# Optimization experiments

Measured on AMD Instinct MI355X. Metric: run time of the kernel, lower is better.

The kernel has to match this reference:

```python
import jax, jax.numpy as jnp
import numpy as np
from math import factorial, sqrt, pi

LMAX, NSH = 2, 9
F = 64
N_RBF = 20
N_INTER = 2
N_ATOMS = 1000
N_PAIRS = 10000
CUTOFF = 5.0

# ---------- Clebsch-Gordan coefficients for real spherical harmonics ----------

def _cg_complex(l1, m1, l2, m2, l3, m3):
    # <l1 m1 l2 m2 | l3 m3> via Racah formula
    if m3 != m1 + m2 or not (abs(l1 - l2) <= l3 <= l1 + l2):
        return 0.0
    f = factorial
    pre = sqrt((2 * l3 + 1) * f(l3 + l1 - l2) * f(l3 - l1 + l2) * f(l1 + l2 - l3) / f(l1 + l2 + l3 + 1))
    pre *= sqrt(f(l3 + m3) * f(l3 - m3) * f(l1 - m1) * f(l1 + m1) * f(l2 - m2) * f(l2 + m2))
    s = 0.0
    for k in range(l1 + l2 - l3 + 1):
        d = [k, l1 + l2 - l3 - k, l1 - m1 - k, l2 + m2 - k, l3 - l2 + m1 + k, l3 - l1 - m2 + k]
        if min(d) < 0:
            continue
        s += (-1) ** k / np.prod([float(f(t)) for t in d])
    return pre * s

def _sh_indices(lmax):
    l = np.concatenate([np.full(2 * ll + 1, ll) for ll in range(lmax + 1)])
    m = np.concatenate([np.arange(-ll, ll + 1) for ll in range(lmax + 1)])
    return l, m

def _real_cg(lmax):
    lidx, midx = _sh_indices(lmax)
    n = (lmax + 1) ** 2
    cgc = np.zeros((n, n, n))
    for a in range(n):
        for b in range(n):
            for c in range(n):
                cgc[a, b, c] = _cg_complex(lidx[a], midx[a], lidx[b], midx[b], lidx[c], midx[c])
    # complex -> real spherical harmonic change of basis (per degree l)
    U = np.zeros((n, n), dtype=np.complex128)
    for ll in range(lmax + 1):
        base = ll * ll + ll
        U[base, base] = 1.0
        for m in range(1, ll + 1):
            U[base + m, base - m] = 1 / sqrt(2)
            U[base + m, base + m] = (-1) ** m / sqrt(2)
            U[base - m, base - m] = 1j / sqrt(2)
            U[base - m, base + m] = -1j * (-1) ** m / sqrt(2)
    cgr = np.einsum('ijk,ai,bj,ck->abc', cgc.astype(np.complex128), U, U, U.conj())
    parity = (-1.0) ** lidx
    mask = (parity[:, None, None] * parity[None, :, None]) == parity[None, None, :]
    cgr = np.real(cgr) * mask
    cgr = np.transpose(cgr, (2, 0, 1))  # [s_out, s_in(x), s_filter(Y)]
    s1, s2, s3 = np.nonzero(np.abs(cgr) > 1e-9)
    return s1, s2, s3, cgr[s1, s2, s3].astype(np.float32), lidx

_S1, _S2, _S3, _CGV, _LIDX = _real_cg(LMAX)
IDX1 = jnp.asarray(_S1)            # output sh channel per CG path
IDX2 = jnp.asarray(_S2)            # input-feature sh channel per CG path
IDX3 = jnp.asarray(_S3)            # Ylm sh channel per CG path
CGVAL = jnp.asarray(_CGV)          # CG value per path
WIDX = jnp.asarray(_LIDX[_S3])     # radial-filter degree per CG path
LIDX = jnp.asarray(_LIDX)          # degree of each of the 9 sh channels

# ---------- real spherical harmonics (lmax=2, orthonormal, m=-l..l order) ----------

def _rsh(u):
    x, y, z = u[:, 0], u[:, 1], u[:, 2]
    c1 = sqrt(3.0 / (4.0 * pi))
    c2 = 0.5 * sqrt(15.0 / pi)
    return jnp.stack([
        jnp.full_like(x, 0.5 / sqrt(pi)),
        c1 * y, c1 * z, c1 * x,
        c2 * x * y,
        c2 * y * z,
        0.25 * sqrt(5.0 / pi) * (3.0 * z * z - 1.0),
        c2 * x * z,
        0.25 * sqrt(15.0 / pi) * (x * x - y * y),
    ], axis=1)


def setup_inputs() -> dict:
    key = jax.random.key(0)
    ks = jax.random.split(key, 10)
    atomic_numbers = jax.random.randint(ks[0], (N_ATOMS,), 0, 100)
    r_ij = 1.5 * jax.random.normal(ks[1], (N_PAIRS, 3), dtype=jnp.float32)
    idx_i = jnp.sort(jax.random.randint(ks[2], (N_PAIRS,), 0, N_ATOMS))
    idx_j = jax.random.randint(ks[3], (N_PAIRS,), 0, N_ATOMS)
    emb = jax.random.normal(ks[4], (100, F), dtype=jnp.float32)
    def s(k, sh, fan):
        return jax.random.normal(k, sh, dtype=jnp.float32) / float(np.sqrt(fan))
    Wf = s(ks[5], (N_INTER, N_RBF, (LMAX + 1) * F), N_RBF)
    bf = jnp.zeros((N_INTER, (LMAX + 1) * F), jnp.float32)
    W1 = s(ks[6], (N_INTER, F, F), F)
    W2 = s(ks[7], (N_INTER, F, F), F)
    W3 = s(ks[8], (N_INTER, F, F), F)
    Wg = s(ks[9], (N_INTER, F, (LMAX + 1) * F), F)
    bg = jnp.zeros((N_INTER, (LMAX + 1) * F), jnp.float32)
    return dict(atomic_numbers=atomic_numbers, r_ij=r_ij, idx_i=idx_i, idx_j=idx_j,
                emb=emb, Wf=Wf, bf=bf, W1=W1, W2=W2, W3=W3, Wg=Wg, bg=bg)


def reference(atomic_numbers, r_ij, idx_i, idx_j, emb, Wf, bf, W1, W2, W3, Wg, bg):
    n_atoms = atomic_numbers.shape[0]
    d = jnp.linalg.norm(r_ij, axis=1, keepdims=True)          # [P,1]
    Yij = _rsh(r_ij / d)                                       # [P,9]
    offsets = jnp.linspace(0.0, CUTOFF, N_RBF)                 # GaussianRBF
    width = CUTOFF / (N_RBF - 1)
    radial = jnp.exp((-0.5 / (width * width)) * (d - offsets) ** 2)   # [P,n_rbf]
    cut = 0.5 * (jnp.cos(d * (pi / CUTOFF)) + 1.0) * (d < CUTOFF)     # [P,1]
    # nuclear embedding + scalar2rsh (zero-pad l>0 channels)
    x = jnp.zeros((n_atoms, NSH, F), emb.dtype).at[:, 0, :].set(emb[atomic_numbers])
    for t in range(N_INTER):
        # SO3Convolution
        Wij = (radial @ Wf[t] + bf[t]).reshape(-1, LMAX + 1, F) * cut[:, :, None]  # [P,lmax+1,F]
        xj = x[idx_j]                                                              # [P,9,F]
        v = xj[:, IDX2] * Yij[:, IDX3, None] * Wij[:, WIDX] * CGVAL[None, :, None]  # [P,nnz,F]
        yij = jnp.zeros_like(xj).at[:, IDX1].add(v)                                 # CG scatter
        dx = jax.ops.segment_sum(yij, idx_i, num_segments=n_atoms)                  # edge->node scatter
        # mixing1 + SO3TensorProduct
        ddx = dx @ W1[t]
        tp = jnp.zeros_like(dx).at[:, IDX1].add(dx[:, IDX2] * ddx[:, IDX3] * CGVAL[None, :, None])
        dx = (dx + tp) @ W2[t]
        # SO3ParametricGatedNonlinearity (gate from l=0 channel)
        gate = (dx[:, 0] @ Wg[t] + bg[t]).reshape(-1, LMAX + 1, F)
        dx = dx * jax.nn.sigmoid(gate[:, LIDX])
        dx = dx @ W3[t]
        x = x + dx
    return x  # multipole_representation [n_atoms, 9, F]; x[:,0] is scalar_representation
```

## Files before the change

### kernel.cpp

```cpp
#include <hip/hip_runtime.h>
#include <cmath>

constexpr int kNsh    = 9;
constexpr int kF      = 64;
constexpr int kNrbf   = 20;
constexpr int kNAtoms = 1000;
constexpr int kNPairs = 10000;
constexpr float kCutoffF = 5.0f;
constexpr int kMaxNZ  = 200;
constexpr int kCp     = 12;
constexpr int kXs     = kF * kCp;

struct CGSparse {
  int n;
  int c[kMaxNZ];
  int a[kMaxNZ];
  int b[kMaxNZ];
  float v[kMaxNZ];
};

constexpr double cfact(int n) {
  double r = 1.0;
  for (int i = 2; i <= n; i++) r *= (double)i;
  return r;
}
constexpr double cabs_(double x) { return x < 0 ? -x : x; }
constexpr double csqrt_(double x) {
  if (x <= 0.0) return 0.0;
  double g = x < 1.0 ? 1.0 : x;
  for (int i = 0; i < 60; i++) g = 0.5 * (g + x / g);
  return g;
}

constexpr double cg_cplx(int l1, int m1, int l2, int m2, int l3, int m3) {
  if (m3 != m1 + m2) return 0.0;
  int lo = l1 > l2 ? l1 - l2 : l2 - l1;
  if (l3 < lo || l3 > l1 + l2) return 0.0;
  double pre = csqrt_((2 * l3 + 1) * cfact(l3 + l1 - l2) * cfact(l3 - l1 + l2) *
                      cfact(l1 + l2 - l3) / cfact(l1 + l2 + l3 + 1));
  pre *= csqrt_(cfact(l3 + m3) * cfact(l3 - m3) * cfact(l1 - m1) *
                cfact(l1 + m1) * cfact(l2 - m2) * cfact(l2 + m2));
  double s = 0.0;
  for (int k = 0; k <= l1 + l2 - l3; k++) {
    int d0 = k, d1 = l1 + l2 - l3 - k, d2 = l1 - m1 - k;
    int d3 = l2 + m2 - k, d4 = l3 - l2 + m1 + k, d5 = l3 - l1 - m2 + k;
    if (d0 < 0 || d1 < 0 || d2 < 0 || d3 < 0 || d4 < 0 || d5 < 0) continue;
    double den = cfact(d0) * cfact(d1) * cfact(d2) * cfact(d3) * cfact(d4) * cfact(d5);
    s += ((k % 2) ? -1.0 : 1.0) / den;
  }
  return pre * s;
}

constexpr CGSparse build_cg() {
  CGSparse out{};
  int lidx[9] = {0, 1, 1, 1, 2, 2, 2, 2, 2};
  int midx[9] = {0, -1, 0, 1, -2, -1, 0, 1, 2};
  double Ur[9][9] = {};
  double Ui[9][9] = {};
  for (int l = 0; l <= 2; l++) {
    int base = l * l + l;
    Ur[base][base] = 1.0;
    for (int m = 1; m <= l; m++) {
      double s2 = 1.0 / csqrt_(2.0);
      double sgn = (m % 2) ? -1.0 : 1.0;
      Ur[base + m][base - m] = s2;
      Ur[base + m][base + m] = sgn * s2;
      Ui[base - m][base - m] = s2;
      Ui[base - m][base + m] = -sgn * s2;
    }
  }
  double cgr[9][9][9] = {};
  for (int i = 0; i < 9; i++)
    for (int j = 0; j < 9; j++)
      for (int k = 0; k < 9; k++) {
        double cv = cg_cplx(lidx[i], midx[i], lidx[j], midx[j], lidx[k], midx[k]);
        if (cv == 0.0) continue;
        for (int a2 = 0; a2 < 9; a2++) {
          if (Ur[a2][i] == 0.0 && Ui[a2][i] == 0.0) continue;
          for (int b2 = 0; b2 < 9; b2++) {
            if (Ur[b2][j] == 0.0 && Ui[b2][j] == 0.0) continue;
            for (int c2 = 0; c2 < 9; c2++) {
              if (Ur[c2][k] == 0.0 && Ui[c2][k] == 0.0) continue;
              double ar = Ur[a2][i], ai = Ui[a2][i];
              double br = Ur[b2][j], bi = Ui[b2][j];
              double cr = Ur[c2][k], ci = -Ui[c2][k];
              double pr = ar * br - ai * bi;
              double pi = ar * bi + ai * br;
              double rr = pr * cr - pi * ci;
              cgr[c2][a2][b2] += rr * cv;
            }
          }
        }
      }
  int n = 0;
  for (int c2 = 0; c2 < 9; c2++)
    for (int a2 = 0; a2 < 9; a2++)
      for (int b2 = 0; b2 < 9; b2++) {
        bool mask = ((lidx[a2] + lidx[b2]) % 2) == (lidx[c2] % 2);
        double v = mask ? cgr[c2][a2][b2] : 0.0;
        if (cabs_(v) > 1e-9) {
          out.c[n] = c2;
          out.a[n] = a2;
          out.b[n] = b2;
          out.v[n] = (float)v;
          n++;
        }
      }
  out.n = n;
  return out;
}

constexpr CGSparse CG = build_cg();
static_assert(CG.n > 0 && CG.n <= kMaxNZ, "CG table size out of range");

constexpr int kPreBlkPairs = kNPairs / 4;
constexpr int kPreBlkSeg   = (kNAtoms + 1 + 255) / 256;
constexpr int kPreBlkTotal = kPreBlkPairs + kPreBlkSeg;

__global__ __launch_bounds__(256) void k_pre(
    const float* __restrict__ rij, const int* __restrict__ idx_i,
    float* __restrict__ pd_all, int* __restrict__ seg) {
  const int blk = blockIdx.x;
  if (blk < kPreBlkPairs) {
    int wv = threadIdx.x >> 6;
    int f = threadIdx.x & 63;
    int p = blk * 4 + wv;
    float rx = rij[3 * p + 0], ry = rij[3 * p + 1], rz = rij[3 * p + 2];
    float d = sqrtf(rx * rx + ry * ry + rz * rz);
    float inv = 1.0f / d;
    float x = rx * inv, y = ry * inv, z = rz * inv;
    const float c0 = 0.28209479177387814f;
    const float c1 = 0.4886025119029199f;
    const float c2 = 1.0925484305920792f;
    const float c3 = 0.31539156525252005f;
    const float c4 = 0.5462742152960396f;
    float cut = (d < kCutoffF) ? 0.5f * (cosf(d * (float)(M_PI / 5.0)) + 1.0f) : 0.0f;
    float val = 0.f;
    if (f < 9) {
      val =
          (f == 0) ? c0 :
          (f == 1) ? c1 * y :
          (f == 2) ? c1 * z :
          (f == 3) ? c1 * x :
          (f == 4) ? c2 * x * y :
          (f == 5) ? c2 * y * z :
          (f == 6) ? c3 * (3.0f * z * z - 1.0f) :
          (f == 7) ? c2 * x * z :
                     c4 * (x * x - y * y);
    } else if (f == 9) {
      val = cut;
    } else if (f < 30) {
      const float width = kCutoffF / (kNrbf - 1);
      const float coef = -0.5f / (width * width);
      float off = (kCutoffF * (f - 10)) / (kNrbf - 1);
      float tt = d - off;
      val = expf(coef * tt * tt) * cut;
    }
    if (f < 30) pd_all[p * 32 + f] = val;
  } else {
    int a = (blk - kPreBlkPairs) * 256 + threadIdx.x;
    if (a <= kNAtoms) {
      int lo = 0, hi = kNPairs;
      while (lo < hi) {
        int mid = (lo + hi) >> 1;
        if (idx_i[mid] < a) lo = mid + 1; else hi = mid;
      }
      seg[a] = lo;
    }
  }
}

__device__ __forceinline__ void mm_phase(const float* __restrict__ sIn,
                                         const float* __restrict__ W,
                                         float* __restrict__ sRw,
                                         int k0, int cgi, int fb) {
  if (cgi >= 3) return;
  const int c0 = cgi * 4;
  float acc[4][4];
  #pragma unroll
  for (int i = 0; i < 4; i++)
    #pragma unroll
    for (int j = 0; j < 4; j++) acc[i][j] = 0.f;
  #pragma unroll
  for (int half = 0; half < 2; half++) {
    float4 wr[8];
    #pragma unroll
    for (int kk = 0; kk < 8; kk++) {
      wr[kk] = *(const float4*)(W + (k0 + half * 8 + kk) * kF + fb);
    }
    #pragma unroll
    for (int kk = 0; kk < 8; kk++) {
      int k = k0 + half * 8 + kk;
      float4 av = *(const float4*)(sIn + k * kCp + c0);
      float4 wv = wr[kk];
      float a[4] = {av.x, av.y, av.z, av.w};
      float w[4] = {wv.x, wv.y, wv.z, wv.w};
      #pragma unroll
      for (int i = 0; i < 4; i++)
        #pragma unroll
        for (int j = 0; j < 4; j++) acc[i][j] += a[i] * w[j];
    }
  }
  #pragma unroll
  for (int j = 0; j < 4; j++) {
    float4 v = {acc[0][j], acc[1][j], acc[2][j], acc[3][j]};
    *(float4*)(sRw + (fb + j) * kCp + c0) = v;
  }
}

template <int T>
__global__ __launch_bounds__(256) void k_inter(
    const float* __restrict__ pd_all, const float* __restrict__ Wft,
    const float* __restrict__ bft, const int* __restrict__ seg,
    const int* __restrict__ idx_j, const int* __restrict__ Z,
    const float* __restrict__ emb, const float* __restrict__ x_in,
    const float* __restrict__ W1, const float* __restrict__ W2,
    const float* __restrict__ W3, const float* __restrict__ Wg,
    const float* __restrict__ bg, float* __restrict__ x_out) {
  const int atom = blockIdx.x;
  const int tid = threadIdx.x;
  const int wv = tid >> 6;
  const int lane = tid & 63;
  const int cgi = lane >> 4;
  const int fb = (lane & 15) * 4;
  const int k0 = wv * 16;

  __shared__ __align__(16) float sWf[kNrbf * 192];
  __shared__ __align__(16) float sA[kF * kCp];
  __shared__ __align__(16) float sR[4][kF * kCp];
  __shared__ __align__(16) float sGp[4][192];

  {
    const float4* g4 = (const float4*)Wft;
    float4* s4 = (float4*)sWf;
    #pragma unroll
    for (int r = 0; r < 4; r++) {
      int i = r * 256 + tid;
      if (i < kNrbf * 192 / 4) s4[i] = g4[i];
    }
  }
  const float bf0 = bft[lane], bf1 = bft[64 + lane], bf2 = bft[128 + lane];
  __syncthreads();

  {
    float y[12];
    #pragma unroll
    for (int c = 0; c < 12; c++) y[c] = 0.f;
    const int s0 = seg[atom], s1 = seg[atom + 1];
    for (int p0 = s0 + wv; p0 < s1; p0 += 4) {
      const int p = __builtin_amdgcn_readfirstlane(p0);
      const int j = __builtin_amdgcn_readfirstlane(idx_j[p]);
      const float* pd = pd_all + p * 32;
      const float cut = pd[9];
      float Wl0 = bf0 * cut, Wl1 = bf1 * cut, Wl2 = bf2 * cut;
      #pragma unroll
      for (int k = 0; k < kNrbf; k++) {
        float r = pd[10 + k];
        Wl0 += r * sWf[k * 192 + lane];
        Wl1 += r * sWf[k * 192 + 64 + lane];
        Wl2 += r * sWf[k * 192 + 128 + lane];
      }
      float YW[9];
      YW[0] = pd[0] * Wl0;
      YW[1] = pd[1] * Wl1;
      YW[2] = pd[2] * Wl1;
      YW[3] = pd[3] * Wl1;
      #pragma unroll
      for (int b = 4; b < 9; b++) YW[b] = pd[b] * Wl2;
      if (T == 0) {
        float e = emb[Z[j] * kF + lane];
        #pragma unroll
        for (int q = 0; q < CG.n; q++) {
          if (CG.a[q] == 0) y[CG.c[q]] += CG.v[q] * YW[CG.b[q]] * e;
        }
      } else {
        const float* xj = x_in + j * kXs + lane * kCp;
        float xv[12];
        *(float4*)&xv[0] = *(const float4*)(xj + 0);
        *(float4*)&xv[4] = *(const float4*)(xj + 4);
        *(float4*)&xv[8] = *(const float4*)(xj + 8);
        #pragma unroll
        for (int q = 0; q < CG.n; q++) {
          y[CG.c[q]] += CG.v[q] * YW[CG.b[q]] * xv[CG.a[q]];
        }
      }
    }
    float4* r4 = (float4*)(sR[wv] + lane * kCp);
    r4[0] = *(float4*)&y[0];
    r4[1] = *(float4*)&y[4];
    r4[2] = *(float4*)&y[8];
  }
  __syncthreads();
  if (tid < 192) {
    const float4* r0 = (const float4*)sR[0];
    const float4* r1 = (const float4*)sR[1];
    const float4* r2 = (const float4*)sR[2];
    const float4* r3 = (const float4*)sR[3];
    float4 a = r0[tid], b = r1[tid], c = r2[tid], d = r3[tid];
    float4 s = {a.x + b.x + c.x + d.x, a.y + b.y + c.y + d.y,
                a.z + b.z + c.z + d.z, a.w + b.w + c.w + d.w};
    ((float4*)sA)[tid] = s;
  }
  __syncthreads();

  mm_phase(sA, W1, sR[wv], k0, cgi, fb);
  __syncthreads();

  if (wv == 0) {
    float dxv[12], ddx[12];
    {
      const float4* sa = (const float4*)(sA + lane * kCp);
      *(float4*)&dxv[0] = sa[0];
      *(float4*)&dxv[4] = sa[1];
      *(float4*)&dxv[8] = sa[2];
    }
    #pragma unroll
    for (int c = 0; c < 12; c++) {
      ddx[c] = sR[0][lane * kCp + c] + sR[1][lane * kCp + c] +
               sR[2][lane * kCp + c] + sR[3][lane * kCp + c];
    }
    float t2[12];
    #pragma unroll
    for (int c = 0; c < 9; c++) t2[c] = dxv[c];
    t2[9] = 0.f; t2[10] = 0.f; t2[11] = 0.f;
    #pragma unroll
    for (int q = 0; q < CG.n; q++) {
      t2[CG.c[q]] += CG.v[q] * dxv[CG.a[q]] * ddx[CG.b[q]];
    }
    float4* sa = (float4*)(sA + lane * kCp);
    sa[0] = *(float4*)&t2[0];
    sa[1] = *(float4*)&t2[4];
    sa[2] = *(float4*)&t2[8];
  }
  __syncthreads();

  mm_phase(sA, W2, sR[wv], k0, cgi, fb);
  __syncthreads();

  {
    float g0 = 0.f, g1 = 0.f, g2 = 0.f;
    #pragma unroll 4
    for (int kk = 0; kk < 16; kk++) {
      int k = k0 + kk;
      float a = sR[0][k * kCp] + sR[1][k * kCp] + sR[2][k * kCp] + sR[3][k * kCp];
      g0 += a * Wg[k * 192 + lane];
      g1 += a * Wg[k * 192 + 64 + lane];
      g2 += a * Wg[k * 192 + 128 + lane];
    }
    sGp[wv][lane] = g0;
    sGp[wv][64 + lane] = g1;
    sGp[wv][128 + lane] = g2;
  }
  __syncthreads();

  if (wv == 0) {
    float dx2v[12];
    #pragma unroll
    for (int c = 0; c < 12; c++) {
      dx2v[c] = sR[0][lane * kCp + c] + sR[1][lane * kCp + c] +
                sR[2][lane * kCp + c] + sR[3][lane * kCp + c];
    }
    float g0 = bg[lane] + sGp[0][lane] + sGp[1][lane] + sGp[2][lane] + sGp[3][lane];
    float g1 = bg[64 + lane] + sGp[0][64 + lane] + sGp[1][64 + lane] +
               sGp[2][64 + lane] + sGp[3][64 + lane];
    float g2 = bg[128 + lane] + sGp[0][128 + lane] + sGp[1][128 + lane] +
               sGp[2][128 + lane] + sGp[3][128 + lane];
    g0 = 1.f / (1.f + expf(-g0));
    g1 = 1.f / (1.f + expf(-g1));
    g2 = 1.f / (1.f + expf(-g2));
    float dx3[12];
    dx3[0] = dx2v[0] * g0;
    dx3[1] = dx2v[1] * g1;
    dx3[2] = dx2v[2] * g1;
    dx3[3] = dx2v[3] * g1;
    #pragma unroll
    for (int c = 4; c < 9; c++) dx3[c] = dx2v[c] * g2;
    dx3[9] = 0.f; dx3[10] = 0.f; dx3[11] = 0.f;
    float4* sa = (float4*)(sA + lane * kCp);
    sa[0] = *(float4*)&dx3[0];
    sa[1] = *(float4*)&dx3[4];
    sa[2] = *(float4*)&dx3[8];
  }
  __syncthreads();

  mm_phase(sA, W3, sR[wv], k0, cgi, fb);
  __syncthreads();

  if (T == 0) {
    if (tid < 192) {
      const int f = tid / 3, r = tid % 3;
      const float4* r0 = (const float4*)sR[0];
      const float4* r1 = (const float4*)sR[1];
      const float4* r2 = (const float4*)sR[2];
      const float4* r3 = (const float4*)sR[3];
      float4 a = r0[tid], b = r1[tid], c = r2[tid], d = r3[tid];
      float4 s = {a.x + b.x + c.x + d.x, a.y + b.y + c.y + d.y,
                  a.z + b.z + c.z + d.z, a.w + b.w + c.w + d.w};
      if (r == 0) s.x += emb[Z[atom] * kF + f];
      *(float4*)(x_out + atom * kXs + tid * 4) = s;
    }
  } else {
    if (tid < 192) {
      const float4* r0 = (const float4*)sR[0];
      const float4* r1 = (const float4*)sR[1];
      const float4* r2 = (const float4*)sR[2];
      const float4* r3 = (const float4*)sR[3];
      float4 a = r0[tid], b = r1[tid], c = r2[tid], d = r3[tid];
      float4 xi = *(const float4*)(x_in + atom * kXs + tid * 4);
      float4 s = {a.x + b.x + c.x + d.x + xi.x, a.y + b.y + c.y + d.y + xi.y,
                  a.z + b.z + c.z + d.z + xi.z, a.w + b.w + c.w + d.w + xi.w};
      ((float4*)sA)[tid] = s;
    }
    __syncthreads();
    #pragma unroll
    for (int r = 0; r < 3; r++) {
      int i = r * 256 + tid;
      if (i < kNsh * kF) {
        int c = i >> 6, f = i & 63;
        x_out[atom * (kNsh * kF) + i] = sA[f * kCp + c];
      }
    }
  }
}

extern "C" void kernel_launch(void* const* d_in, const int* in_sizes, int n_in,
                              void* d_out, int out_size, void* d_ws, size_t ws_size,
                              hipStream_t stream) {
  const int* Z        = (const int*)d_in[0];
  const float* rij    = (const float*)d_in[1];
  const int* idx_i    = (const int*)d_in[2];
  const int* idx_j    = (const int*)d_in[3];
  const float* emb    = (const float*)d_in[4];
  const float* Wf     = (const float*)d_in[5];
  const float* bf     = (const float*)d_in[6];
  const float* W1     = (const float*)d_in[7];
  const float* W2     = (const float*)d_in[8];
  const float* W3     = (const float*)d_in[9];
  const float* Wg     = (const float*)d_in[10];
  const float* bg     = (const float*)d_in[11];
  float* out = (float*)d_out;

  float* x1  = (float*)d_ws;
  float* pd  = x1 + kNAtoms * kXs;
  int*   seg = (int*)(pd + kNPairs * 32);

  k_pre<<<kPreBlkTotal, 256, 0, stream>>>(rij, idx_i, pd, seg);

  k_inter<0><<<kNAtoms, 256, 0, stream>>>(
      pd, Wf, bf, seg, idx_j, Z, emb, x1,
      W1, W2, W3, Wg, bg, x1);

  k_inter<1><<<kNAtoms, 256, 0, stream>>>(
      pd, Wf + kNrbf * 192, bf + 192, seg, idx_j, Z, emb, x1,
      W1 + kF * kF, W2 + kF * kF, W3 + kF * kF,
      Wg + kF * 192, bg + 192, out);
}
```

Before: 123.9 us.

## Precompute per-pair radial filter weights for both interactions in the pre kernel

Moves the radial filter matmul (RBF times Wf plus bias, scaled by cutoff) out of both interaction kernels into extra blocks of the pre kernel. These blocks write a per-pair 192-wide weight buffer for each of the two interactions into workspace. The interaction kernels now read three floats per lane per pair instead of staging Wf in shared memory and doing a 20-term FMA loop. The cost is about 15 MB of extra global traffic for writing and reading pairW. The extra blocks also recompute the RBF values redundantly.

```diff
diff --git a/kernel.cpp b/kernel.cpp
--- a/kernel.cpp
+++ b/kernel.cpp
@@ -115,11 +115,16 @@
 
 constexpr int kPreBlkPairs = kNPairs / 4;
 constexpr int kPreBlkSeg   = (kNAtoms + 1 + 255) / 256;
-constexpr int kPreBlkTotal = kPreBlkPairs + kPreBlkSeg;
+constexpr int kFiltPPW     = 10;
+constexpr int kFiltWaves   = 2 * kNPairs / kFiltPPW;
+constexpr int kFiltBlocks  = kFiltWaves / 4;
+constexpr int kPreBlkTotal = kPreBlkPairs + kPreBlkSeg + kFiltBlocks;
 
 __global__ __launch_bounds__(256) void k_pre(
     const float* __restrict__ rij, const int* __restrict__ idx_i,
-    float* __restrict__ pd_all, int* __restrict__ seg) {
+    const float* __restrict__ Wf, const float* __restrict__ bf,
+    float* __restrict__ pd_all, float* __restrict__ pairW,
+    int* __restrict__ seg) {
   const int blk = blockIdx.x;
   if (blk < kPreBlkPairs) {
     int wv = threadIdx.x >> 6;
@@ -157,7 +162,7 @@
       val = expf(coef * tt * tt) * cut;
     }
     if (f < 30) pd_all[p * 32 + f] = val;
-  } else {
+  } else if (blk < kPreBlkPairs + kPreBlkSeg) {
     int a = (blk - kPreBlkPairs) * 256 + threadIdx.x;
     if (a <= kNAtoms) {
       int lo = 0, hi = kNPairs;
@@ -166,6 +171,44 @@
         if (idx_i[mid] < a) lo = mid + 1; else hi = mid;
       }
       seg[a] = lo;
+    }
+  } else {
+    const int wid = (blk - kPreBlkPairs - kPreBlkSeg) * 4 + (threadIdx.x >> 6);
+    const int lane = threadIdx.x & 63;
+    const int t = wid / (kFiltWaves / 2);
+    const int chunk = wid % (kFiltWaves / 2);
+    const float* Wft = Wf + t * kNrbf * 192;
+    float w0r[kNrbf], w1r[kNrbf], w2r[kNrbf];
+    #pragma unroll
+    for (int k = 0; k < kNrbf; k++) {
+      w0r[k] = Wft[k * 192 + lane];
+      w1r[k] = Wft[k * 192 + 64 + lane];
+      w2r[k] = Wft[k * 192 + 128 + lane];
+    }
+    const float b0 = bf[t * 192 + lane];
+    const float b1 = bf[t * 192 + 64 + lane];
+    const float b2 = bf[t * 192 + 128 + lane];
+    float* outt = pairW + t * kNPairs * 192;
+    const float width = kCutoffF / (kNrbf - 1);
+    const float coef = -0.5f / (width * width);
+    for (int i = 0; i < kFiltPPW; i++) {
+      const int p = __builtin_amdgcn_readfirstlane(chunk * kFiltPPW + i);
+      float rx = rij[3 * p + 0], ry = rij[3 * p + 1], rz = rij[3 * p + 2];
+      float d = sqrtf(rx * rx + ry * ry + rz * rz);
+      float cut = (d < kCutoffF) ? 0.5f * (cosf(d * (float)(M_PI / 5.0)) + 1.0f) : 0.0f;
+      float a0 = b0 * cut, a1 = b1 * cut, a2 = b2 * cut;
+      #pragma unroll
+      for (int k = 0; k < kNrbf; k++) {
+        float off = (kCutoffF * k) / (kNrbf - 1);
+        float tt = d - off;
+        float r = expf(coef * tt * tt) * cut;
+        a0 += r * w0r[k];
+        a1 += r * w1r[k];
+        a2 += r * w2r[k];
+      }
+      outt[p * 192 + lane] = a0;
+      outt[p * 192 + 64 + lane] = a1;
+      outt[p * 192 + 128 + lane] = a2;
     }
   }
 }
@@ -210,10 +253,10 @@
 
 template <int T>
 __global__ __launch_bounds__(256) void k_inter(
-    const float* __restrict__ pd_all, const float* __restrict__ Wft,
-    const float* __restrict__ bft, const int* __restrict__ seg,
-    const int* __restrict__ idx_j, const int* __restrict__ Z,
-    const float* __restrict__ emb, const float* __restrict__ x_in,
+    const float* __restrict__ pd_all, const float* __restrict__ pairW,
+    const int* __restrict__ seg, const int* __restrict__ idx_j,
+    const int* __restrict__ Z, const float* __restrict__ emb,
+    const float* __restrict__ x_in,
     const float* __restrict__ W1, const float* __restrict__ W2,
     const float* __restrict__ W3, const float* __restrict__ Wg,
     const float* __restrict__ bg, float* __restrict__ x_out) {
@@ -225,22 +268,9 @@
   const int fb = (lane & 15) * 4;
   const int k0 = wv * 16;
 
-  __shared__ __align__(16) float sWf[kNrbf * 192];
   __shared__ __align__(16) float sA[kF * kCp];
   __shared__ __align__(16) float sR[4][kF * kCp];
   __shared__ __align__(16) float sGp[4][192];
-
-  {
-    const float4* g4 = (const float4*)Wft;
-    float4* s4 = (float4*)sWf;
-    #pragma unroll
-    for (int r = 0; r < 4; r++) {
-      int i = r * 256 + tid;
-      if (i < kNrbf * 192 / 4) s4[i] = g4[i];
-    }
-  }
-  const float bf0 = bft[lane], bf1 = bft[64 + lane], bf2 = bft[128 + lane];
-  __syncthreads();
 
   {
     float y[12];
@@ -251,15 +281,10 @@
       const int p = __builtin_amdgcn_readfirstlane(p0);
       const int j = __builtin_amdgcn_readfirstlane(idx_j[p]);
       const float* pd = pd_all + p * 32;
-      const float cut = pd[9];
-      float Wl0 = bf0 * cut, Wl1 = bf1 * cut, Wl2 = bf2 * cut;
-      #pragma unroll
-      for (int k = 0; k < kNrbf; k++) {
-        float r = pd[10 + k];
-        Wl0 += r * sWf[k * 192 + lane];
-        Wl1 += r * sWf[k * 192 + 64 + lane];
-        Wl2 += r * sWf[k * 192 + 128 + lane];
-      }
+      const float* wp = pairW + p * 192;
+      float Wl0 = wp[lane];
+      float Wl1 = wp[64 + lane];
+      float Wl2 = wp[128 + lane];
       float YW[9];
       YW[0] = pd[0] * Wl0;
       YW[1] = pd[1] * Wl1;
@@ -442,16 +467,17 @@
 
   float* x1  = (float*)d_ws;
   float* pd  = x1 + kNAtoms * kXs;
-  int*   seg = (int*)(pd + kNPairs * 32);
-
-  k_pre<<<kPreBlkTotal, 256, 0, stream>>>(rij, idx_i, pd, seg);
+  float* pw  = pd + kNPairs * 32;
+  int*   seg = (int*)(pw + 2 * kNPairs * 192);
+
+  k_pre<<<kPreBlkTotal, 256, 0, stream>>>(rij, idx_i, Wf, bf, pd, pw, seg);
 
   k_inter<0><<<kNAtoms, 256, 0, stream>>>(
-      pd, Wf, bf, seg, idx_j, Z, emb, x1,
+      pd, pw, seg, idx_j, Z, emb, x1,
       W1, W2, W3, Wg, bg, x1);
 
   k_inter<1><<<kNAtoms, 256, 0, stream>>>(
-      pd, Wf + kNrbf * 192, bf + 192, seg, idx_j, Z, emb, x1,
+      pd, pw + kNPairs * 192, seg, idx_j, Z, emb, x1,
       W1 + kF * kF, W2 + kF * kF, W3 + kF * kF,
       Wg + kF * 192, bg + 192, out);
 }
```

Result: slower. 139.7 us (+12.7%).

## Fuse pair preprocessing into per-atom kernel and shrink blocks to one wave

Applied to the files above, without the earlier changes.

Removes the separate preprocessing kernel: each atom block now does its own segment binary search and computes spherical harmonics, cutoff and radial basis for its pairs in LDS chunks, recomputing them in both interaction launches. Blocks drop from four waves to one 64-thread wave with radial filter weights held in registers, and the dense mixing matmuls stream weights per feature instead of splitting work across waves and reducing partials. This cuts one launch, the pd workspace round trip and the cross-wave reductions and syncs, at the cost of less parallelism per atom, more registers and duplicated geometry work.

```diff
diff --git a/kernel.cpp b/kernel.cpp
--- a/kernel.cpp
+++ b/kernel.cpp
@@ -10,6 +10,8 @@
 constexpr int kMaxNZ  = 200;
 constexpr int kCp     = 12;
 constexpr int kXs     = kF * kCp;
+constexpr int kChunk  = 32;
+constexpr int kPdS    = 36;
 
 struct CGSparse {
   int n;
@@ -113,152 +115,123 @@
 constexpr CGSparse CG = build_cg();
 static_assert(CG.n > 0 && CG.n <= kMaxNZ, "CG table size out of range");
 
-constexpr int kPreBlkPairs = kNPairs / 4;
-constexpr int kPreBlkSeg   = (kNAtoms + 1 + 255) / 256;
-constexpr int kPreBlkTotal = kPreBlkPairs + kPreBlkSeg;
-
-__global__ __launch_bounds__(256) void k_pre(
+__device__ __forceinline__ void mm_stream(const float* __restrict__ sDx,
+                                          const float* __restrict__ W,
+                                          int f, float* __restrict__ acc) {
+  #pragma unroll
+  for (int c = 0; c < 9; c++) acc[c] = 0.f;
+  #pragma unroll 4
+  for (int kq = 0; kq < 16; kq++) {
+    float w0 = W[(4 * kq + 0) * kF + f];
+    float w1 = W[(4 * kq + 1) * kF + f];
+    float w2 = W[(4 * kq + 2) * kF + f];
+    float w3 = W[(4 * kq + 3) * kF + f];
+    #pragma unroll
+    for (int c = 0; c < 9; c++) {
+      float4 dv = *(const float4*)(sDx + c * kF + 4 * kq);
+      acc[c] += dv.x * w0 + dv.y * w1 + dv.z * w2 + dv.w * w3;
+    }
+  }
+}
+
+template <int T>
+__global__ __launch_bounds__(64) void k_so3(
     const float* __restrict__ rij, const int* __restrict__ idx_i,
-    float* __restrict__ pd_all, int* __restrict__ seg) {
-  const int blk = blockIdx.x;
-  if (blk < kPreBlkPairs) {
-    int wv = threadIdx.x >> 6;
-    int f = threadIdx.x & 63;
-    int p = blk * 4 + wv;
-    float rx = rij[3 * p + 0], ry = rij[3 * p + 1], rz = rij[3 * p + 2];
-    float d = sqrtf(rx * rx + ry * ry + rz * rz);
-    float inv = 1.0f / d;
-    float x = rx * inv, y = ry * inv, z = rz * inv;
-    const float c0 = 0.28209479177387814f;
-    const float c1 = 0.4886025119029199f;
-    const float c2 = 1.0925484305920792f;
-    const float c3 = 0.31539156525252005f;
-    const float c4 = 0.5462742152960396f;
-    float cut = (d < kCutoffF) ? 0.5f * (cosf(d * (float)(M_PI / 5.0)) + 1.0f) : 0.0f;
-    float val = 0.f;
-    if (f < 9) {
-      val =
-          (f == 0) ? c0 :
-          (f == 1) ? c1 * y :
-          (f == 2) ? c1 * z :
-          (f == 3) ? c1 * x :
-          (f == 4) ? c2 * x * y :
-          (f == 5) ? c2 * y * z :
-          (f == 6) ? c3 * (3.0f * z * z - 1.0f) :
-          (f == 7) ? c2 * x * z :
-                     c4 * (x * x - y * y);
-    } else if (f == 9) {
-      val = cut;
-    } else if (f < 30) {
-      const float width = kCutoffF / (kNrbf - 1);
-      const float coef = -0.5f / (width * width);
-      float off = (kCutoffF * (f - 10)) / (kNrbf - 1);
-      float tt = d - off;
-      val = expf(coef * tt * tt) * cut;
-    }
-    if (f < 30) pd_all[p * 32 + f] = val;
-  } else {
-    int a = (blk - kPreBlkPairs) * 256 + threadIdx.x;
-    if (a <= kNAtoms) {
-      int lo = 0, hi = kNPairs;
-      while (lo < hi) {
-        int mid = (lo + hi) >> 1;
-        if (idx_i[mid] < a) lo = mid + 1; else hi = mid;
-      }
-      seg[a] = lo;
-    }
-  }
-}
-
-__device__ __forceinline__ void mm_phase(const float* __restrict__ sIn,
-                                         const float* __restrict__ W,
-                                         float* __restrict__ sRw,
-                                         int k0, int cgi, int fb) {
-  if (cgi >= 3) return;
-  const int c0 = cgi * 4;
-  float acc[4][4];
-  #pragma unroll
-  for (int i = 0; i < 4; i++)
-    #pragma unroll
-    for (int j = 0; j < 4; j++) acc[i][j] = 0.f;
-  #pragma unroll
-  for (int half = 0; half < 2; half++) {
-    float4 wr[8];
-    #pragma unroll
-    for (int kk = 0; kk < 8; kk++) {
-      wr[kk] = *(const float4*)(W + (k0 + half * 8 + kk) * kF + fb);
-    }
-    #pragma unroll
-    for (int kk = 0; kk < 8; kk++) {
-      int k = k0 + half * 8 + kk;
-      float4 av = *(const float4*)(sIn + k * kCp + c0);
-      float4 wv = wr[kk];
-      float a[4] = {av.x, av.y, av.z, av.w};
-      float w[4] = {wv.x, wv.y, wv.z, wv.w};
-      #pragma unroll
-      for (int i = 0; i < 4; i++)
-        #pragma unroll
-        for (int j = 0; j < 4; j++) acc[i][j] += a[i] * w[j];
-    }
-  }
-  #pragma unroll
-  for (int j = 0; j < 4; j++) {
-    float4 v = {acc[0][j], acc[1][j], acc[2][j], acc[3][j]};
-    *(float4*)(sRw + (fb + j) * kCp + c0) = v;
-  }
-}
-
-template <int T>
-__global__ __launch_bounds__(256) void k_inter(
-    const float* __restrict__ pd_all, const float* __restrict__ Wft,
-    const float* __restrict__ bft, const int* __restrict__ seg,
     const int* __restrict__ idx_j, const int* __restrict__ Z,
-    const float* __restrict__ emb, const float* __restrict__ x_in,
-    const float* __restrict__ W1, const float* __restrict__ W2,
-    const float* __restrict__ W3, const float* __restrict__ Wg,
-    const float* __restrict__ bg, float* __restrict__ x_out) {
+    const float* __restrict__ emb, const float* __restrict__ Wft,
+    const float* __restrict__ bft, const float* __restrict__ W1,
+    const float* __restrict__ W2, const float* __restrict__ W3,
+    const float* __restrict__ Wg, const float* __restrict__ bg,
+    const float* __restrict__ x_in, float* __restrict__ x_out) {
   const int atom = blockIdx.x;
-  const int tid = threadIdx.x;
-  const int wv = tid >> 6;
-  const int lane = tid & 63;
-  const int cgi = lane >> 4;
-  const int fb = (lane & 15) * 4;
-  const int k0 = wv * 16;
-
-  __shared__ __align__(16) float sWf[kNrbf * 192];
-  __shared__ __align__(16) float sA[kF * kCp];
-  __shared__ __align__(16) float sR[4][kF * kCp];
-  __shared__ __align__(16) float sGp[4][192];
-
+  const int f = threadIdx.x;
+
+  __shared__ __align__(16) float pdLDS[kChunk * kPdS];
+  __shared__ __align__(16) float dxLDS[kNsh * kF];
+  __shared__ __align__(16) float rowLDS[kF];
+
+  float w0r[kNrbf], w1r[kNrbf], w2r[kNrbf];
+  #pragma unroll
+  for (int k = 0; k < kNrbf; k++) {
+    w0r[k] = Wft[k * 192 + f];
+    w1r[k] = Wft[k * 192 + 64 + f];
+    w2r[k] = Wft[k * 192 + 128 + f];
+  }
+  const float bf0 = bft[f], bf1 = bft[64 + f], bf2 = bft[128 + f];
+
+  int lo = 0;
   {
-    const float4* g4 = (const float4*)Wft;
-    float4* s4 = (float4*)sWf;
-    #pragma unroll
-    for (int r = 0; r < 4; r++) {
-      int i = r * 256 + tid;
-      if (i < kNrbf * 192 / 4) s4[i] = g4[i];
-    }
-  }
-  const float bf0 = bft[lane], bf1 = bft[64 + lane], bf2 = bft[128 + lane];
-  __syncthreads();
-
-  {
-    float y[12];
-    #pragma unroll
-    for (int c = 0; c < 12; c++) y[c] = 0.f;
-    const int s0 = seg[atom], s1 = seg[atom + 1];
-    for (int p0 = s0 + wv; p0 < s1; p0 += 4) {
-      const int p = __builtin_amdgcn_readfirstlane(p0);
-      const int j = __builtin_amdgcn_readfirstlane(idx_j[p]);
-      const float* pd = pd_all + p * 32;
+    const int a = atom + (f & 1);
+    int hi = kNPairs;
+    while (lo < hi) {
+      int mid = (lo + hi) >> 1;
+      if (idx_i[mid] < a) lo = mid + 1; else hi = mid;
+    }
+  }
+  const int s0 = __builtin_amdgcn_readlane(lo, 0);
+  const int s1 = __builtin_amdgcn_readlane(lo, 1);
+
+  float y[9];
+  #pragma unroll
+  for (int c = 0; c < 9; c++) y[c] = 0.f;
+
+  for (int cb = s0; cb < s1; cb += kChunk) {
+    const int cn = (s1 - cb < kChunk) ? (s1 - cb) : kChunk;
+    for (int item = f; item < cn * 32; item += 64) {
+      const int pp = item >> 5, slot = item & 31;
+      const int p = cb + pp;
+      float rx = rij[3 * p + 0], ry = rij[3 * p + 1], rz = rij[3 * p + 2];
+      float d = sqrtf(rx * rx + ry * ry + rz * rz);
+      float inv = 1.0f / d;
+      float ux = rx * inv, uy = ry * inv, uz = rz * inv;
+      const float c0 = 0.28209479177387814f;
+      const float c1 = 0.4886025119029199f;
+      const float c2 = 1.0925484305920792f;
+      const float c3 = 0.31539156525252005f;
+      const float c4 = 0.5462742152960396f;
+      float cut = (d < kCutoffF) ? 0.5f * (cosf(d * (float)(M_PI / 5.0)) + 1.0f) : 0.0f;
+      float val;
+      if (slot < 9) {
+        val =
+            (slot == 0) ? c0 :
+            (slot == 1) ? c1 * uy :
+            (slot == 2) ? c1 * uz :
+            (slot == 3) ? c1 * ux :
+            (slot == 4) ? c2 * ux * uy :
+            (slot == 5) ? c2 * uy * uz :
+            (slot == 6) ? c3 * (3.0f * uz * uz - 1.0f) :
+            (slot == 7) ? c2 * ux * uz :
+                          c4 * (ux * ux - uy * uy);
+      } else if (slot == 9) {
+        val = cut;
+      } else if (slot >= 12) {
+        const float width = kCutoffF / (kNrbf - 1);
+        const float coef = -0.5f / (width * width);
+        float off = (kCutoffF * (slot - 12)) / (kNrbf - 1);
+        float tt = d - off;
+        val = expf(coef * tt * tt) * cut;
+      } else {
+        continue;
+      }
+      pdLDS[pp * kPdS + slot] = val;
+    }
+    __syncthreads();
+
+    for (int pp = 0; pp < cn; pp++) {
+      const int p = cb + pp;
+      const int j = idx_j[p];
+      const float* pd = pdLDS + pp * kPdS;
       const float cut = pd[9];
       float Wl0 = bf0 * cut, Wl1 = bf1 * cut, Wl2 = bf2 * cut;
       #pragma unroll
-      for (int k = 0; k < kNrbf; k++) {
-        float r = pd[10 + k];
-        Wl0 += r * sWf[k * 192 + lane];
-        Wl1 += r * sWf[k * 192 + 64 + lane];
-        Wl2 += r * sWf[k * 192 + 128 + lane];
+      for (int kq = 0; kq < 5; kq++) {
+        float4 r4 = *(const float4*)(pd + 12 + 4 * kq);
+        Wl0 += r4.x * w0r[4 * kq] + r4.y * w0r[4 * kq + 1] +
+               r4.z * w0r[4 * kq + 2] + r4.w * w0r[4 * kq + 3];
+        Wl1 += r4.x * w1r[4 * kq] + r4.y * w1r[4 * kq + 1] +
+               r4.z * w1r[4 * kq + 2] + r4.w * w1r[4 * kq + 3];
+        Wl2 += r4.x * w2r[4 * kq] + r4.y * w2r[4 * kq + 1] +
+               r4.z * w2r[4 * kq + 2] + r4.w * w2r[4 * kq + 3];
       }
       float YW[9];
       YW[0] = pd[0] * Wl0;
@@ -268,13 +241,13 @@
       #pragma unroll
       for (int b = 4; b < 9; b++) YW[b] = pd[b] * Wl2;
       if (T == 0) {
-        float e = emb[Z[j] * kF + lane];
+        float e = emb[Z[j] * kF + f];
         #pragma unroll
         for (int q = 0; q < CG.n; q++) {
           if (CG.a[q] == 0) y[CG.c[q]] += CG.v[q] * YW[CG.b[q]] * e;
         }
       } else {
-        const float* xj = x_in + j * kXs + lane * kCp;
+        const float* xj = x_in + j * kXs + f * kCp;
         float xv[12];
         *(float4*)&xv[0] = *(const float4*)(xj + 0);
         *(float4*)&xv[4] = *(const float4*)(xj + 4);
@@ -285,140 +258,84 @@
         }
       }
     }
-    float4* r4 = (float4*)(sR[wv] + lane * kCp);
-    r4[0] = *(float4*)&y[0];
-    r4[1] = *(float4*)&y[4];
-    r4[2] = *(float4*)&y[8];
-  }
-  __syncthreads();
-  if (tid < 192) {
-    const float4* r0 = (const float4*)sR[0];
-    const float4* r1 = (const float4*)sR[1];
-    const float4* r2 = (const float4*)sR[2];
-    const float4* r3 = (const float4*)sR[3];
-    float4 a = r0[tid], b = r1[tid], c = r2[tid], d = r3[tid];
-    float4 s = {a.x + b.x + c.x + d.x, a.y + b.y + c.y + d.y,
-                a.z + b.z + c.z + d.z, a.w + b.w + c.w + d.w};
-    ((float4*)sA)[tid] = s;
-  }
-  __syncthreads();
-
-  mm_phase(sA, W1, sR[wv], k0, cgi, fb);
-  __syncthreads();
-
-  if (wv == 0) {
-    float dxv[12], ddx[12];
-    {
-      const float4* sa = (const float4*)(sA + lane * kCp);
-      *(float4*)&dxv[0] = sa[0];
-      *(float4*)&dxv[4] = sa[1];
-      *(float4*)&dxv[8] = sa[2];
-    }
+    __syncthreads();
+  }
+
+  #pragma unroll
+  for (int c = 0; c < 9; c++) dxLDS[c * kF + f] = y[c];
+  __syncthreads();
+  float ddx[9];
+  mm_stream(dxLDS, W1, f, ddx);
+
+  float t2[9];
+  #pragma unroll
+  for (int c = 0; c < 9; c++) t2[c] = y[c];
+  #pragma unroll
+  for (int q = 0; q < CG.n; q++) {
+    t2[CG.c[q]] += CG.v[q] * y[CG.a[q]] * ddx[CG.b[q]];
+  }
+
+  __syncthreads();
+  #pragma unroll
+  for (int c = 0; c < 9; c++) dxLDS[c * kF + f] = t2[c];
+  __syncthreads();
+  float dx2[9];
+  mm_stream(dxLDS, W2, f, dx2);
+
+  rowLDS[f] = dx2[0];
+  __syncthreads();
+  float g0 = bg[f], g1 = bg[64 + f], g2 = bg[128 + f];
+  #pragma unroll 4
+  for (int kq = 0; kq < 16; kq++) {
+    float4 a4 = *(const float4*)(rowLDS + 4 * kq);
+    float av[4] = {a4.x, a4.y, a4.z, a4.w};
     #pragma unroll
-    for (int c = 0; c < 12; c++) {
-      ddx[c] = sR[0][lane * kCp + c] + sR[1][lane * kCp + c] +
-               sR[2][lane * kCp + c] + sR[3][lane * kCp + c];
-    }
-    float t2[12];
+    for (int qq = 0; qq < 4; qq++) {
+      const int k = 4 * kq + qq;
+      g0 += av[qq] * Wg[k * 192 + f];
+      g1 += av[qq] * Wg[k * 192 + 64 + f];
+      g2 += av[qq] * Wg[k * 192 + 128 + f];
+    }
+  }
+  g0 = 1.f / (1.f + expf(-g0));
+  g1 = 1.f / (1.f + expf(-g1));
+  g2 = 1.f / (1.f + expf(-g2));
+
+  float dx3[9];
+  dx3[0] = dx2[0] * g0;
+  dx3[1] = dx2[1] * g1;
+  dx3[2] = dx2[2] * g1;
+  dx3[3] = dx2[3] * g1;
+  #pragma unroll
+  for (int c = 4; c < 9; c++) dx3[c] = dx2[c] * g2;
+
+  __syncthreads();
+  #pragma unroll
+  for (int c = 0; c < 9; c++) dxLDS[c * kF + f] = dx3[c];
+  __syncthreads();
+  float o[9];
+  mm_stream(dxLDS, W3, f, o);
+
+  if (T == 0) {
+    float r0 = emb[Z[atom] * kF + f];
+    float buf[12];
     #pragma unroll
-    for (int c = 0; c < 9; c++) t2[c] = dxv[c];
-    t2[9] = 0.f; t2[10] = 0.f; t2[11] = 0.f;
+    for (int c = 0; c < 9; c++) buf[c] = o[c];
+    buf[0] += r0;
+    buf[9] = 0.f; buf[10] = 0.f; buf[11] = 0.f;
+    float* dst = x_out + atom * kXs + f * kCp;
+    *(float4*)(dst + 0) = *(float4*)&buf[0];
+    *(float4*)(dst + 4) = *(float4*)&buf[4];
+    *(float4*)(dst + 8) = *(float4*)&buf[8];
+  } else {
+    const float* xi = x_in + atom * kXs + f * kCp;
+    float xv[12];
+    *(float4*)&xv[0] = *(const float4*)(xi + 0);
+    *(float4*)&xv[4] = *(const float4*)(xi + 4);
+    *(float4*)&xv[8] = *(const float4*)(xi + 8);
     #pragma unroll
-    for (int q = 0; q < CG.n; q++) {
-      t2[CG.c[q]] += CG.v[q] * dxv[CG.a[q]] * ddx[CG.b[q]];
-    }
-    float4* sa = (float4*)(sA + lane * kCp);
-    sa[0] = *(float4*)&t2[0];
-    sa[1] = *(float4*)&t2[4];
-    sa[2] = *(float4*)&t2[8];
-  }
-  __syncthreads();
-
-  mm_phase(sA, W2, sR[wv], k0, cgi, fb);
-  __syncthreads();
-
-  {
-    float g0 = 0.f, g1 = 0.f, g2 = 0.f;
-    #pragma unroll 4
-    for (int kk = 0; kk < 16; kk++) {
-      int k = k0 + kk;
-      float a = sR[0][k * kCp] + sR[1][k * kCp] + sR[2][k * kCp] + sR[3][k * kCp];
-      g0 += a * Wg[k * 192 + lane];
-      g1 += a * Wg[k * 192 + 64 + lane];
-      g2 += a * Wg[k * 192 + 128 + lane];
-    }
-    sGp[wv][lane] = g0;
-    sGp[wv][64 + lane] = g1;
-    sGp[wv][128 + lane] = g2;
-  }
-  __syncthreads();
-
-  if (wv == 0) {
-    float dx2v[12];
-    #pragma unroll
-    for (int c = 0; c < 12; c++) {
-      dx2v[c] = sR[0][lane * kCp + c] + sR[1][lane * kCp + c] +
-                sR[2][lane * kCp + c] + sR[3][lane * kCp + c];
-    }
-    float g0 = bg[lane] + sGp[0][lane] + sGp[1][lane] + sGp[2][lane] + sGp[3][lane];
-    float g1 = bg[64 + lane] + sGp[0][64 + lane] + sGp[1][64 + lane] +
-               sGp[2][64 + lane] + sGp[3][64 + lane];
-    float g2 = bg[128 + lane] + sGp[0][128 + lane] + sGp[1][128 + lane] +
-               sGp[2][128 + lane] + sGp[3][128 + lane];
-    g0 = 1.f / (1.f + expf(-g0));
-    g1 = 1.f / (1.f + expf(-g1));
-    g2 = 1.f / (1.f + expf(-g2));
-    float dx3[12];
-    dx3[0] = dx2v[0] * g0;
-    dx3[1] = dx2v[1] * g1;
-    dx3[2] = dx2v[2] * g1;
-    dx3[3] = dx2v[3] * g1;
-    #pragma unroll
-    for (int c = 4; c < 9; c++) dx3[c] = dx2v[c] * g2;
-    dx3[9] = 0.f; dx3[10] = 0.f; dx3[11] = 0.f;
-    float4* sa = (float4*)(sA + lane * kCp);
-    sa[0] = *(float4*)&dx3[0];
-    sa[1] = *(float4*)&dx3[4];
-    sa[2] = *(float4*)&dx3[8];
-  }
-  __syncthreads();
-
-  mm_phase(sA, W3, sR[wv], k0, cgi, fb);
-  __syncthreads();
-
-  if (T == 0) {
-    if (tid < 192) {
-      const int f = tid / 3, r = tid % 3;
-      const float4* r0 = (const float4*)sR[0];
-      const float4* r1 = (const float4*)sR[1];
-      const float4* r2 = (const float4*)sR[2];
-      const float4* r3 = (const float4*)sR[3];
-      float4 a = r0[tid], b = r1[tid], c = r2[tid], d = r3[tid];
-      float4 s = {a.x + b.x + c.x + d.x, a.y + b.y + c.y + d.y,
-                  a.z + b.z + c.z + d.z, a.w + b.w + c.w + d.w};
-      if (r == 0) s.x += emb[Z[atom] * kF + f];
-      *(float4*)(x_out + atom * kXs + tid * 4) = s;
-    }
-  } else {
-    if (tid < 192) {
-      const float4* r0 = (const float4*)sR[0];
-      const float4* r1 = (const float4*)sR[1];
-      const float4* r2 = (const float4*)sR[2];
-      const float4* r3 = (const float4*)sR[3];
-      float4 a = r0[tid], b = r1[tid], c = r2[tid], d = r3[tid];
-      float4 xi = *(const float4*)(x_in + atom * kXs + tid * 4);
-      float4 s = {a.x + b.x + c.x + d.x + xi.x, a.y + b.y + c.y + d.y + xi.y,
-                  a.z + b.z + c.z + d.z + xi.z, a.w + b.w + c.w + d.w + xi.w};
-      ((float4*)sA)[tid] = s;
-    }
-    __syncthreads();
-    #pragma unroll
-    for (int r = 0; r < 3; r++) {
-      int i = r * 256 + tid;
-      if (i < kNsh * kF) {
-        int c = i >> 6, f = i & 63;
-        x_out[atom * (kNsh * kF) + i] = sA[f * kCp + c];
-      }
+    for (int c = 0; c < 9; c++) {
+      x_out[atom * (kNsh * kF) + c * kF + f] = o[c] + xv[c];
     }
   }
 }
@@ -440,18 +357,14 @@
   const float* bg     = (const float*)d_in[11];
   float* out = (float*)d_out;
 
-  float* x1  = (float*)d_ws;
-  float* pd  = x1 + kNAtoms * kXs;
-  int*   seg = (int*)(pd + kNPairs * 32);
-
-  k_pre<<<kPreBlkTotal, 256, 0, stream>>>(rij, idx_i, pd, seg);
-
-  k_inter<0><<<kNAtoms, 256, 0, stream>>>(
-      pd, Wf, bf, seg, idx_j, Z, emb, x1,
-      W1, W2, W3, Wg, bg, x1);
-
-  k_inter<1><<<kNAtoms, 256, 0, stream>>>(
-      pd, Wf + kNrbf * 192, bf + 192, seg, idx_j, Z, emb, x1,
+  float* x1 = (float*)d_ws;
+
+  k_so3<0><<<kNAtoms, 64, 0, stream>>>(
+      rij, idx_i, idx_j, Z, emb, Wf, bf,
+      W1, W2, W3, Wg, bg, (const float*)nullptr, x1);
+
+  k_so3<1><<<kNAtoms, 64, 0, stream>>>(
+      rij, idx_i, idx_j, Z, emb, Wf + kNrbf * 192, bf + 192,
       W1 + kF * kF, W2 + kF * kF, W3 + kF * kF,
-      Wg + kF * 192, bg + 192, out);
-}
+      Wg + kF * 192, bg + 192, x1, out);
+}
```

Result: slower. 152.5 us (+23.1%).
